# Kernel tuning notes

Measured on AMD Instinct MI355X. Metric: run time of the kernel, lower is better.

The kernel has to match this reference:

```python
import jax, jax.numpy as jnp
import numpy as np

D_MODEL = 768
NUM_HEADS = 12
D_K = D_MODEL // NUM_HEADS


def setup_inputs() -> dict:
    key = jax.random.key(0)
    ks = jax.random.split(key, 7)
    B, S = 4, 2048
    query = jax.random.normal(ks[0], (B, S, D_MODEL), dtype=jnp.float32)
    key_t = jax.random.normal(ks[1], (B, S, D_MODEL), dtype=jnp.float32)
    value = jax.random.normal(ks[2], (B, S, D_MODEL), dtype=jnp.float32)
    lim = 1.0 / np.sqrt(D_MODEL)
    Wq = jax.random.uniform(ks[3], (D_MODEL, D_MODEL), jnp.float32, -lim, lim)  # torch Linear weight [out,in]
    bq = jax.random.uniform(ks[4], (D_MODEL,), jnp.float32, -lim, lim)
    Wo = jax.random.uniform(ks[5], (D_MODEL, D_MODEL), jnp.float32, -lim, lim)
    bo = jax.random.uniform(ks[6], (D_MODEL,), jnp.float32, -lim, lim)
    return {"query": query, "key": key_t, "value": value,
            "Wq": Wq, "bq": bq, "Wo": Wo, "bo": bo}


def _proj_heads(x, W, b):
    # x: [B,S,D] -> [B,H,S,d_k]; torch Linear: x @ W.T + b
    B, S, _ = x.shape
    y = x @ W.T + b
    return y.reshape(B, S, NUM_HEADS, D_K).transpose(0, 2, 1, 3)


def reference(query, key, value, Wq, bq, Wo, bo):
    # Faithful to source: linear_q is used for q, k AND v (source bug).
    q = _proj_heads(query, Wq, bq)
    k = _proj_heads(key, Wq, bq)
    v = _proj_heads(value, Wq, bq)
    scale = 1.0 / jnp.sqrt(jnp.asarray(D_K, q.dtype))
    scores = jnp.einsum('bhqd,bhkd->bhqk', q, k) * scale  # [B,H,S,S]
    attn = jax.nn.softmax(scores, axis=-1)
    out = jnp.einsum('bhqk,bhkd->bhqd', attn, v)  # [B,H,S,d_k]
    B, H, S, dk = out.shape
    out = out.transpose(0, 2, 1, 3).reshape(B, S, H * dk)
    return out @ Wo.T + bo
```

## Files before the change

### kernel.cpp

```cpp
#include <hip/hip_runtime.h>
#include <math.h>

typedef _Float16 f16x8 __attribute__((ext_vector_type(8)));
typedef _Float16 f16x4 __attribute__((ext_vector_type(4)));
typedef float    f32x4 __attribute__((ext_vector_type(4)));
typedef unsigned short us4 __attribute__((ext_vector_type(4)));
typedef unsigned int u32;
typedef unsigned int u32x4 __attribute__((ext_vector_type(4)));

constexpr int DM = 768, NH = 12, DK = 64, SEQ = 2048, BB = 4;
constexpr int MROWS = BB * SEQ;
constexpr size_t XELE = (size_t)MROWS * DM;
constexpr size_t WELE = (size_t)DM * DM;

constexpr size_t OFF_X16  = 0;
constexpr size_t OFF_W16  = 3 * XELE;
constexpr size_t OFF_WO16 = OFF_W16 + WELE;
constexpr size_t OFF_QKV  = OFF_WO16 + WELE;
constexpr size_t OFF_ATT  = OFF_QKV + 3 * XELE;
constexpr size_t TOT_CVTW = 2 * WELE;


constexpr float QSCALE = 0.125f * 1.44269504f;
constexpr float MSEED = -8.0f;

__device__ __forceinline__ void gload16(const _Float16* g, _Float16* l) {
    __builtin_amdgcn_global_load_lds(
        (const __attribute__((address_space(1))) unsigned int*)g,
        (__attribute__((address_space(3))) unsigned int*)l, 16, 0, 0);
}

__device__ __forceinline__ uint2 pack4(float a, float b, float c, float d) {
    uint2 r;
    r.x = __builtin_bit_cast(u32, __builtin_amdgcn_cvt_pkrtz(a, b));
    r.y = __builtin_bit_cast(u32, __builtin_amdgcn_cvt_pkrtz(c, d));
    return r;
}

__global__ __launch_bounds__(256) void cvt_w(
    const float* __restrict__ wq, const float* __restrict__ wo,
    _Float16* __restrict__ dst)
{
    const size_t i = ((size_t)blockIdx.x * 256 + threadIdx.x) * 4;
    if (i >= TOT_CVTW) return;
    const float* src = (i < WELE) ? wq : wo;
    const size_t base = (i < WELE) ? 0 : WELE;
    const float4 f = *(const float4*)(src + (i - base));
    _Float16 h4[4] = {(_Float16)f.x, (_Float16)f.y, (_Float16)f.z, (_Float16)f.w};
    *(us4*)(dst + i) = *(us4*)h4;
}

__global__ __launch_bounds__(256) void gemm_qkv(
    const float* __restrict__ q32, const float* __restrict__ k32,
    const float* __restrict__ v32, const _Float16* __restrict__ Wmat,
    const float* __restrict__ bias, _Float16* __restrict__ Yout)
{
    __shared__ _Float16 smem[128 * 136];

    const int bid = blockIdx.x;
    const int xs  = bid & 7;
    const int rr  = bid >> 3;
    const int m_blk = ((rr & 7) << 3) | xs;
    const int tt  = rr >> 3;
    const int n_blk = tt % 6;
    const int z     = tt / 6;

    const int tid  = threadIdx.x;
    const int w    = tid >> 6, lane = tid & 63;
    const int cl   = lane & 15;
    const int g    = lane >> 4;
    const int m0   = m_blk * 128, n0 = n_blk * 128;
    const float* Xf = (z == 0) ? q32 : (z == 1) ? k32 : v32;

    const int wr = w >> 1, wc = w & 1;
    const int lrow = lane >> 2;
    const int lcol = (lane & 3) * 8;

    f32x4 acc[4][4] = {};

    constexpr int NK = DM / 32;

    {
        float4 av[2][2];
#pragma unroll
        for (int t = 0; t < 2; ++t) {
            const int c = w + t * 4;
            const float* srcA = Xf + (size_t)(m0 + c * 16 + lrow) * DM + lcol;
            av[t][0] = *(const float4*)srcA;
            av[t][1] = *(const float4*)(srcA + 4);
            gload16(Wmat + (size_t)(n0 + c * 16 + lrow) * DM + lcol, &smem[4096 + c * 512]);
        }
#pragma unroll
        for (int t = 0; t < 2; ++t) {
            const int c = w + t * 4;
            _Float16 h8[8] = {
                (_Float16)av[t][0].x, (_Float16)av[t][0].y,
                (_Float16)av[t][0].z, (_Float16)av[t][0].w,
                (_Float16)av[t][1].x, (_Float16)av[t][1].y,
                (_Float16)av[t][1].z, (_Float16)av[t][1].w};
            *(f16x8*)&smem[c * 512 + lane * 8] = *(f16x8*)h8;
        }
    }

    int cur = 0;
    for (int ki = 0; ki < NK; ++ki) {
        __syncthreads();
        const bool pre = (ki + 1 < NK);
        float4 av[2][2];
        if (pre) {
            const int kn = (ki + 1) * 32;
            _Float16* dst = &smem[(cur ^ 1) * 8192];
#pragma unroll
            for (int t = 0; t < 2; ++t) {
                const int c = w + t * 4;
                const float* srcA = Xf + (size_t)(m0 + c * 16 + lrow) * DM + kn + lcol;
                av[t][0] = *(const float4*)srcA;
                av[t][1] = *(const float4*)(srcA + 4);
                gload16(Wmat + (size_t)(n0 + c * 16 + lrow) * DM + kn + lcol, &dst[4096 + c * 512]);
            }
        }

        const _Float16* As = &smem[cur * 8192];
        const _Float16* Bs = As + 4096;

        f16x8 a[4], bfr[4];
#pragma unroll
        for (int mt = 0; mt < 4; ++mt)
            a[mt] = *(const f16x8*)&As[(wr * 64 + mt * 16 + cl) * 32 + g * 8];
#pragma unroll
        for (int nt = 0; nt < 4; ++nt)
            bfr[nt] = *(const f16x8*)&Bs[(wc * 64 + nt * 16 + cl) * 32 + g * 8];
#pragma unroll
        for (int mt = 0; mt < 4; ++mt)
#pragma unroll
            for (int nt = 0; nt < 4; ++nt)
                acc[mt][nt] = __builtin_amdgcn_mfma_f32_16x16x32_f16(
                    a[mt], bfr[nt], acc[mt][nt], 0, 0, 0);

        if (pre) {
            _Float16* dst = &smem[(cur ^ 1) * 8192];
#pragma unroll
            for (int t = 0; t < 2; ++t) {
                const int c = w + t * 4;
                _Float16 h8[8] = {
                    (_Float16)av[t][0].x, (_Float16)av[t][0].y,
                    (_Float16)av[t][0].z, (_Float16)av[t][0].w,
                    (_Float16)av[t][1].x, (_Float16)av[t][1].y,
                    (_Float16)av[t][1].z, (_Float16)av[t][1].w};
                *(f16x8*)&dst[c * 512 + lane * 8] = *(f16x8*)h8;
            }
        }
        cur ^= 1;
    }

    __syncthreads();
    const float sc = (z == 0) ? QSCALE : 1.0f;
#pragma unroll
    for (int nt = 0; nt < 4; ++nt) {
        const int col = wc * 64 + nt * 16 + cl;
        const float bv = bias[n0 + col];
#pragma unroll
        for (int mt = 0; mt < 4; ++mt)
#pragma unroll
            for (int r = 0; r < 4; ++r) {
                const int row = wr * 64 + mt * 16 + g * 4 + r;
                const _Float16 hv = (_Float16)((acc[mt][nt][r] + bv) * sc);
                if (z == 2) smem[col * 136 + row] = hv;
                else        smem[row * 136 + col] = hv;
            }
    }
    __syncthreads();

    _Float16* Yz = Yout + (size_t)z * XELE;
#pragma unroll
    for (int it = 0; it < 8; ++it) {
        const int idx = tid + it * 256;
        const int row = idx >> 4;
        const int grp = idx & 15;
        const f16x8 vv = *(const f16x8*)&smem[row * 136 + grp * 8];
        if (z == 2) {
            const int f  = n0 + row, hh = f >> 6, d = f & 63;
            const int gm = m0 + grp * 8;
            const int bb = gm >> 11, s = gm & (SEQ - 1);
            const int ssw = (s & ~63) | ((((s >> 3) & 7) ^ (d & 7)) << 3);
            *(f16x8*)&Yz[(((size_t)bb * NH + hh) * DK + d) * SEQ + ssw] = vv;
        } else {
            const int gm = m0 + row;
            const int bb = gm >> 11, s = gm & (SEQ - 1);
            const int n  = n0 + grp * 8, hh = n >> 6, d0 = n & 63;
            const int dsw = ((((d0 >> 3) ^ (s & 7)) & 7) << 3);
            *(f16x8*)&Yz[(((size_t)bb * NH + hh) * SEQ + s) * DK + dsw] = vv;
        }
    }
}

__global__ __launch_bounds__(256) void gemm_out(
    const _Float16* __restrict__ X,
    const _Float16* __restrict__ Wmat,
    const float* __restrict__ bias, float* __restrict__ Y)
{
    __shared__ _Float16 smem[2 * 6144];

    const int bid = blockIdx.x;
    const int xs  = bid & 7;
    const int rr  = bid >> 3;
    const int m_blk = ((rr & 15) << 3) | xs;
    const int n_blk = rr >> 4;

    const int tid = threadIdx.x;
    const int w = tid >> 6, lane = tid & 63;
    const int cl = lane & 15, g = lane >> 4;
    const int m0 = m_blk * 64, n0 = n_blk * 128;

    const int lrow = lane >> 2;
    const int lcol = (lane & 3) * 8;

    f32x4 acc[4][2] = {};

    constexpr int NK = DM / 32;
    gload16(X    + (size_t)(m0 + w * 16 + lrow) * DM + lcol, &smem[w * 512]);
    gload16(Wmat + (size_t)(n0 + w * 16 + lrow) * DM + lcol, &smem[2048 + w * 512]);
    gload16(Wmat + (size_t)(n0 + (w + 4) * 16 + lrow) * DM + lcol, &smem[2048 + (w + 4) * 512]);

    int cur = 0;
    for (int ki = 0; ki < NK; ++ki) {
        __syncthreads();
        if (ki + 1 < NK) {
            const int kn = (ki + 1) * 32;
            _Float16* dst = &smem[(cur ^ 1) * 6144];
            gload16(X    + (size_t)(m0 + w * 16 + lrow) * DM + kn + lcol, &dst[w * 512]);
            gload16(Wmat + (size_t)(n0 + w * 16 + lrow) * DM + kn + lcol, &dst[2048 + w * 512]);
            gload16(Wmat + (size_t)(n0 + (w + 4) * 16 + lrow) * DM + kn + lcol, &dst[2048 + (w + 4) * 512]);
        }
        const _Float16* As = &smem[cur * 6144];
        const _Float16* Bs = As + 2048;

        f16x8 a[4], bfr[2];
#pragma unroll
        for (int mt = 0; mt < 4; ++mt)
            a[mt] = *(const f16x8*)&As[(mt * 16 + cl) * 32 + g * 8];
#pragma unroll
        for (int nt = 0; nt < 2; ++nt)
            bfr[nt] = *(const f16x8*)&Bs[(w * 32 + nt * 16 + cl) * 32 + g * 8];
#pragma unroll
        for (int mt = 0; mt < 4; ++mt)
#pragma unroll
            for (int nt = 0; nt < 2; ++nt)
                acc[mt][nt] = __builtin_amdgcn_mfma_f32_16x16x32_f16(
                    a[mt], bfr[nt], acc[mt][nt], 0, 0, 0);
        cur ^= 1;
    }

#pragma unroll
    for (int nt = 0; nt < 2; ++nt) {
        const int col = n0 + w * 32 + nt * 16 + cl;
        const float bv = bias[col];
#pragma unroll
        for (int mt = 0; mt < 4; ++mt)
#pragma unroll
            for (int r = 0; r < 4; ++r) {
                const int row = m0 + mt * 16 + g * 4 + r;
                Y[(size_t)row * DM + col] = acc[mt][nt][r] + bv;
            }
    }
}

__global__ __launch_bounds__(256) void flash4(
    const _Float16* __restrict__ qkv, _Float16* __restrict__ attno)
{
    __shared__ _Float16 KsB[2 * 64 * 64];
    __shared__ _Float16 VtB[2 * 64 * 64];

    const int bid = blockIdx.x;
    const int xs  = bid & 7;
    const int rr  = bid >> 3;
    const int p   = (rr % 6) * 8 + xs;
    const int qtb = rr / 6;
    const int h   = p % NH, b = p / NH;
    const int q0  = qtb * 128;

    const int tid = threadIdx.x;
    const int w = tid >> 6, lane = tid & 63;
    const int cl = lane & 15, g = lane >> 4;
    const int swz = cl & 7;

    const size_t headoff = ((size_t)b * NH + h) * SEQ * DK;
    const _Float16* Qg = qkv + headoff;
    const _Float16* Kg = qkv + XELE + headoff;
    const _Float16* Vg = qkv + 2 * XELE + headoff;

    const int ldr = lane >> 3, ldc = (lane & 7) * 8;

#pragma unroll
    for (int t = 0; t < 2; ++t) {
        const int c = w * 2 + t;
        gload16(Kg + (size_t)(c * 8 + ldr) * DK + ldc, &KsB[c * 512]);
        gload16(Vg + (size_t)(c * 8 + ldr) * SEQ + ldc, &VtB[c * 512]);
    }

    f16x8 qf[2][2];
#pragma unroll
    for (int qt = 0; qt < 2; ++qt)
#pragma unroll
        for (int ks = 0; ks < 2; ++ks)
            qf[qt][ks] = *(const f16x8*)(
                Qg + (size_t)(q0 + w * 32 + qt * 16 + cl) * DK
                   + (((ks * 4 + g) ^ swz) << 3));

    float l_run[2] = {0.f, 0.f};
    f32x4 acc[2][4] = {};

    int cur = 0;
    for (int j0 = 0; j0 < SEQ; j0 += 64) {
        __syncthreads();
        if (j0 + 64 < SEQ) {
            const int jn = j0 + 64;
            _Float16* Kd = &KsB[(cur ^ 1) * 4096];
            _Float16* Vd = &VtB[(cur ^ 1) * 4096];
#pragma unroll
            for (int t = 0; t < 2; ++t) {
                const int c = w * 2 + t;
                gload16(Kg + (size_t)(jn + c * 8 + ldr) * DK + ldc, &Kd[c * 512]);
                gload16(Vg + (size_t)(c * 8 + ldr) * SEQ + jn + ldc, &Vd[c * 512]);
            }
        }
        const _Float16* Ks = &KsB[cur * 4096];
        const _Float16* Vt = &VtB[cur * 4096];

        f16x8 kf[4][2];
#pragma unroll
        for (int kt = 0; kt < 4; ++kt)
#pragma unroll
            for (int ks = 0; ks < 2; ++ks)
                kf[kt][ks] = *(const f16x8*)&Ks[(kt * 16 + cl) * 64
                                                + (((ks * 4 + g) ^ swz) << 3)];

        uint2 pk[2][4];
#pragma unroll
        for (int qt = 0; qt < 2; ++qt) {
            float ps = 0.f;
#pragma unroll
            for (int kt = 0; kt < 4; ++kt) {
                f32x4 s = {MSEED, MSEED, MSEED, MSEED};
#pragma unroll
                for (int ks = 0; ks < 2; ++ks)
                    s = __builtin_amdgcn_mfma_f32_16x16x32_f16(
                        kf[kt][ks], qf[qt][ks], s, 0, 0, 0);
                const float p0 = __builtin_amdgcn_exp2f(s[0]);
                const float p1 = __builtin_amdgcn_exp2f(s[1]);
                const float p2 = __builtin_amdgcn_exp2f(s[2]);
                const float p3 = __builtin_amdgcn_exp2f(s[3]);
                ps += (p0 + p1) + (p2 + p3);
                pk[qt][kt] = pack4(p0, p1, p2, p3);
            }
            l_run[qt] += ps;
        }

        f16x8 pf[2][2];
#pragma unroll
        for (int qt = 0; qt < 2; ++qt)
#pragma unroll
            for (int ks = 0; ks < 2; ++ks) {
                u32 a0 = pk[qt][2 * ks].x, b0 = pk[qt][2 * ks + 1].x;
                u32 a1 = pk[qt][2 * ks].y, b1 = pk[qt][2 * ks + 1].y;
                {
                    auto r = __builtin_amdgcn_permlane32_swap(a0, b0, false, false);
                    a0 = r[0]; b0 = r[1];
                }
                {
                    auto r = __builtin_amdgcn_permlane16_swap(a0, b0, false, false);
                    a0 = r[0]; b0 = r[1];
                }
                {
                    auto r = __builtin_amdgcn_permlane32_swap(a1, b1, false, false);
                    a1 = r[0]; b1 = r[1];
                }
                {
                    auto r = __builtin_amdgcn_permlane16_swap(a1, b1, false, false);
                    a1 = r[0]; b1 = r[1];
                }
                u32x4 wds = {a0, a1, b0, b1};
                pf[qt][ks] = __builtin_bit_cast(f16x8, wds);
            }

        f16x8 vf[4][2];
#pragma unroll
        for (int dt = 0; dt < 4; ++dt)
#pragma unroll
            for (int ks = 0; ks < 2; ++ks)
                vf[dt][ks] = *(const f16x8*)&Vt[(dt * 16 + cl) * 64
                                                + (((ks * 4 + g) ^ swz) << 3)];
#pragma unroll
        for (int qt = 0; qt < 2; ++qt)
#pragma unroll
            for (int ks = 0; ks < 2; ++ks)
#pragma unroll
                for (int dt = 0; dt < 4; ++dt)
                    acc[qt][dt] = __builtin_amdgcn_mfma_f32_16x16x32_f16(
                        vf[dt][ks], pf[qt][ks], acc[qt][dt], 0, 0, 0);
        cur ^= 1;
    }

#pragma unroll
    for (int qt = 0; qt < 2; ++qt) {
        float l = l_run[qt];
        l += __shfl_xor(l, 16);
        l += __shfl_xor(l, 32);
        const float inv = 1.0f / l;
        const int q = q0 + w * 32 + qt * 16 + cl;
#pragma unroll
        for (int dt = 0; dt < 4; ++dt) {
            uint2 pk2 = pack4(acc[qt][dt][0] * inv, acc[qt][dt][1] * inv,
                              acc[qt][dt][2] * inv, acc[qt][dt][3] * inv);
            *(uint2*)&attno[((size_t)b * SEQ + q) * DM + h * DK + dt * 16 + g * 4] = pk2;
        }
    }
}

extern "C" void kernel_launch(void* const* d_in, const int* in_sizes, int n_in,
                              void* d_out, int out_size, void* d_ws, size_t ws_size,
                              hipStream_t stream) {
    const float* q  = (const float*)d_in[0];
    const float* k  = (const float*)d_in[1];
    const float* v  = (const float*)d_in[2];
    const float* Wq = (const float*)d_in[3];
    const float* bq = (const float*)d_in[4];
    const float* Wo = (const float*)d_in[5];
    const float* bo = (const float*)d_in[6];

    _Float16* ws16  = (_Float16*)d_ws;
    _Float16* w16   = ws16 + OFF_W16;
    _Float16* wo16  = ws16 + OFF_WO16;
    _Float16* qkv16 = ws16 + OFF_QKV;
    _Float16* att16 = ws16 + OFF_ATT;

    cvt_w<<<(int)(TOT_CVTW / 1024), 256, 0, stream>>>(Wq, Wo, w16);

    gemm_qkv<<<1152, 256, 0, stream>>>(q, k, v, w16, bq, qkv16);

    flash4<<<768, 256, 0, stream>>>(qkv16, att16);

    gemm_out<<<768, 256, 0, stream>>>(att16, wo16, bo, (float*)d_out);
}
```

Baseline: 275.6 us.

## Deepen QKV projection GEMM prefetch with register-staged A two steps ahead

Restructures the projection GEMM main loop so the fp32 activation tile is loaded into registers two k-steps ahead, while the fp16 conversion and LDS store for the next buffer happen right after the barrier. Explicit s_waitcnt vmcnt/lgkmcnt plus a raw s_barrier replace __syncthreads so the outstanding global loads can keep flying across the barrier. The aim is to hide global-load latency behind the MFMA work. It relies on hand-counted vmcnt values (vmcnt(4)) matching the compiler's instruction order, which is fragile and could cause races if the order differs.

```diff
diff --git a/kernel.cpp b/kernel.cpp
--- a/kernel.cpp
+++ b/kernel.cpp
@@ -13,7 +13,6 @@
 constexpr size_t XELE = (size_t)MROWS * DM;
 constexpr size_t WELE = (size_t)DM * DM;
 
-constexpr size_t OFF_X16  = 0;
 constexpr size_t OFF_W16  = 3 * XELE;
 constexpr size_t OFF_WO16 = OFF_W16 + WELE;
 constexpr size_t OFF_QKV  = OFF_WO16 + WELE;
@@ -79,65 +78,44 @@
     f32x4 acc[4][4] = {};
 
     constexpr int NK = DM / 32;
-
-    {
-        float4 av[2][2];
-#pragma unroll
-        for (int t = 0; t < 2; ++t) {
-            const int c = w + t * 4;
-            const float* srcA = Xf + (size_t)(m0 + c * 16 + lrow) * DM + lcol;
-            av[t][0] = *(const float4*)srcA;
-            av[t][1] = *(const float4*)(srcA + 4);
-            gload16(Wmat + (size_t)(n0 + c * 16 + lrow) * DM + lcol, &smem[4096 + c * 512]);
-        }
-#pragma unroll
-        for (int t = 0; t < 2; ++t) {
-            const int c = w + t * 4;
-            _Float16 h8[8] = {
-                (_Float16)av[t][0].x, (_Float16)av[t][0].y,
-                (_Float16)av[t][0].z, (_Float16)av[t][0].w,
-                (_Float16)av[t][1].x, (_Float16)av[t][1].y,
-                (_Float16)av[t][1].z, (_Float16)av[t][1].w};
-            *(f16x8*)&smem[c * 512 + lane * 8] = *(f16x8*)h8;
-        }
-    }
+    float4 av[2][2];
+
+#pragma unroll
+    for (int t = 0; t < 2; ++t) {
+        const int c = w + t * 4;
+        const float* srcA = Xf + (size_t)(m0 + c * 16 + lrow) * DM + lcol;
+        av[t][0] = *(const float4*)srcA;
+        av[t][1] = *(const float4*)(srcA + 4);
+        gload16(Wmat + (size_t)(n0 + c * 16 + lrow) * DM + lcol, &smem[4096 + c * 512]);
+    }
+#pragma unroll
+    for (int t = 0; t < 2; ++t) {
+        const int c = w + t * 4;
+        _Float16 h8[8] = {
+            (_Float16)av[t][0].x, (_Float16)av[t][0].y,
+            (_Float16)av[t][0].z, (_Float16)av[t][0].w,
+            (_Float16)av[t][1].x, (_Float16)av[t][1].y,
+            (_Float16)av[t][1].z, (_Float16)av[t][1].w};
+        *(f16x8*)&smem[c * 512 + lane * 8] = *(f16x8*)h8;
+    }
+    asm volatile("" ::: "memory");
+#pragma unroll
+    for (int t = 0; t < 2; ++t) {
+        const int c = w + t * 4;
+        const float* srcA = Xf + (size_t)(m0 + c * 16 + lrow) * DM + 32 + lcol;
+        av[t][0] = *(const float4*)srcA;
+        av[t][1] = *(const float4*)(srcA + 4);
+    }
+    asm volatile("" ::: "memory");
 
     int cur = 0;
     for (int ki = 0; ki < NK; ++ki) {
-        __syncthreads();
-        const bool pre = (ki + 1 < NK);
-        float4 av[2][2];
-        if (pre) {
-            const int kn = (ki + 1) * 32;
-            _Float16* dst = &smem[(cur ^ 1) * 8192];
-#pragma unroll
-            for (int t = 0; t < 2; ++t) {
-                const int c = w + t * 4;
-                const float* srcA = Xf + (size_t)(m0 + c * 16 + lrow) * DM + kn + lcol;
-                av[t][0] = *(const float4*)srcA;
-                av[t][1] = *(const float4*)(srcA + 4);
-                gload16(Wmat + (size_t)(n0 + c * 16 + lrow) * DM + kn + lcol, &dst[4096 + c * 512]);
-            }
-        }
-
-        const _Float16* As = &smem[cur * 8192];
-        const _Float16* Bs = As + 4096;
-
-        f16x8 a[4], bfr[4];
-#pragma unroll
-        for (int mt = 0; mt < 4; ++mt)
-            a[mt] = *(const f16x8*)&As[(wr * 64 + mt * 16 + cl) * 32 + g * 8];
-#pragma unroll
-        for (int nt = 0; nt < 4; ++nt)
-            bfr[nt] = *(const f16x8*)&Bs[(wc * 64 + nt * 16 + cl) * 32 + g * 8];
-#pragma unroll
-        for (int mt = 0; mt < 4; ++mt)
-#pragma unroll
-            for (int nt = 0; nt < 4; ++nt)
-                acc[mt][nt] = __builtin_amdgcn_mfma_f32_16x16x32_f16(
-                    a[mt], bfr[nt], acc[mt][nt], 0, 0, 0);
-
-        if (pre) {
+        if (ki + 1 < NK) asm volatile("s_waitcnt vmcnt(4) lgkmcnt(0)" ::: "memory");
+        else             asm volatile("s_waitcnt vmcnt(0) lgkmcnt(0)" ::: "memory");
+        __builtin_amdgcn_s_barrier();
+        asm volatile("" ::: "memory");
+
+        if (ki + 1 < NK) {
             _Float16* dst = &smem[(cur ^ 1) * 8192];
 #pragma unroll
             for (int t = 0; t < 2; ++t) {
@@ -149,7 +127,43 @@
                     (_Float16)av[t][1].z, (_Float16)av[t][1].w};
                 *(f16x8*)&dst[c * 512 + lane * 8] = *(f16x8*)h8;
             }
-        }
+            const int kn = (ki + 1) * 32;
+#pragma unroll
+            for (int t = 0; t < 2; ++t) {
+                const int c = w + t * 4;
+                gload16(Wmat + (size_t)(n0 + c * 16 + lrow) * DM + kn + lcol,
+                        &dst[4096 + c * 512]);
+            }
+            asm volatile("" ::: "memory");
+            if (ki + 2 < NK) {
+                const int kn2 = (ki + 2) * 32;
+#pragma unroll
+                for (int t = 0; t < 2; ++t) {
+                    const int c = w + t * 4;
+                    const float* srcA = Xf + (size_t)(m0 + c * 16 + lrow) * DM + kn2 + lcol;
+                    av[t][0] = *(const float4*)srcA;
+                    av[t][1] = *(const float4*)(srcA + 4);
+                }
+            }
+            asm volatile("" ::: "memory");
+        }
+
+        const _Float16* As = &smem[cur * 8192];
+        const _Float16* Bs = As + 4096;
+
+        f16x8 a[4], bfr[4];
+#pragma unroll
+        for (int mt = 0; mt < 4; ++mt)
+            a[mt] = *(const f16x8*)&As[(wr * 64 + mt * 16 + cl) * 32 + g * 8];
+#pragma unroll
+        for (int nt = 0; nt < 4; ++nt)
+            bfr[nt] = *(const f16x8*)&Bs[(wc * 64 + nt * 16 + cl) * 32 + g * 8];
+#pragma unroll
+        for (int mt = 0; mt < 4; ++mt)
+#pragma unroll
+            for (int nt = 0; nt < 4; ++nt)
+                acc[mt][nt] = __builtin_amdgcn_mfma_f32_16x16x32_f16(
+                    a[mt], bfr[nt], acc[mt][nt], 0, 0, 0);
         cur ^= 1;
     }
 
```

Measured after the change: 262.5 us. 4.7% less time.
